# Optimization experiments

Measured on AMD Instinct MI355X. Metric: run time of the kernel, lower is better.

Reference implementation:

```python
import jax, jax.numpy as jnp
import numpy as np

D_MODEL, D_STATE, V_RANGE, IMG, K = 64, 16, 1, 32, 3
GROUPS = 4
EPS = 1e-5


def _gather_indices():
    H = W = IMG
    v_list = [(x, y) for x in range(-V_RANGE, V_RANGE + 1) for y in range(-V_RANGE, V_RANGE + 1)]
    idx = []
    yg, xg = np.meshgrid(np.arange(H), np.arange(W), indexing='ij')
    for vx, vy in v_list:
        src_y = (yg - vy) % H
        src_x = (xg - vx) % W
        idx.append((src_y * W + src_x).reshape(-1))
    return jnp.asarray(np.stack(idx, axis=0), dtype=jnp.int32)  # (V, H*W)


def setup_inputs() -> dict:
    key = jax.random.key(0)
    ks = jax.random.split(key, 8)
    B = 4
    V = (2 * V_RANGE + 1) ** 2
    fan = D_MODEL * K * K
    std = 1.0 / np.sqrt(fan)
    return {
        'u_t': jax.random.normal(ks[0], (B, D_MODEL, IMG, IMG), jnp.float32),
        's_prev': jax.random.normal(ks[1], (B, V, D_MODEL, D_STATE, IMG, IMG), jnp.float32),
        'gamma': jnp.ones((D_MODEL,), jnp.float32),
        'beta': jnp.zeros((D_MODEL,), jnp.float32),
        'w_delta': jax.random.uniform(ks[2], (D_MODEL, D_MODEL, K, K), jnp.float32, -std, std),
        'b_delta': jax.random.uniform(ks[3], (D_MODEL,), jnp.float32, -std, std),
        'w_B': jax.random.uniform(ks[4], (D_STATE, D_MODEL, K, K), jnp.float32, -std, std),
        'w_C': jax.random.uniform(ks[5], (D_STATE, D_MODEL, K, K), jnp.float32, -std, std),
        'log_A_real': jnp.log(0.5 * jnp.ones((D_MODEL, D_STATE), jnp.float32)),
        'D_param': jnp.ones((D_MODEL,), jnp.float32),
        'dt_inv_softplus': jnp.asarray(np.log(np.exp(1.0) - 1.0), jnp.float32),
        'gather_indices': _gather_indices(),
    }


def _group_norm(x, gamma, beta):
    B, D, H, W = x.shape
    xg = x.reshape(B, GROUPS, D // GROUPS, H, W)
    mu = xg.mean(axis=(2, 3, 4), keepdims=True)
    var = xg.var(axis=(2, 3, 4), keepdims=True)
    xn = ((xg - mu) / jnp.sqrt(var + EPS)).reshape(B, D, H, W)
    return xn * gamma[None, :, None, None] + beta[None, :, None, None]


def _circ_conv(x, w, b=None):
    p = K // 2
    xp = jnp.pad(x, ((0, 0), (0, 0), (p, p), (p, p)), mode='wrap')
    y = jax.lax.conv_general_dilated(xp, w, (1, 1), 'VALID',
                                     dimension_numbers=('NCHW', 'OIHW', 'NCHW'))
    if b is not None:
        y = y + b[None, :, None, None]
    return y


def reference(u_t, s_prev, gamma, beta, w_delta, b_delta, w_B, w_C,
              log_A_real, D_param, dt_inv_softplus, gather_indices):
    B, D, H, W = u_t.shape
    Bv, V, _, N, _, _ = s_prev.shape
    u_norm = _group_norm(u_t, gamma, beta)
    delta = jax.nn.softplus(_circ_conv(u_norm, w_delta, b_delta) + dt_inv_softplus)
    delta = jnp.clip(delta, 1e-4, 5.0)                      # (B,D,H,W)
    B_val = _circ_conv(u_norm, w_B)                          # (B,N,H,W)
    C_val = _circ_conv(u_norm, w_C)                          # (B,N,H,W)
    A = -jnp.exp(log_A_real)                                 # (D,N)
    A_bar = jnp.exp(delta[:, :, None] * A[None, :, :, None, None])  # (B,D,N,H,W)
    B_bar = delta[:, :, None] * B_val[:, None]               # (B,D,N,H,W)
    # flow transport: per-velocity periodic-shift gather over flattened HW
    s_flat = s_prev.reshape(B, V, D, N, H * W)
    s_trans = jax.vmap(lambda sv, iv: jnp.take(sv, iv, axis=-1),
                       in_axes=(1, 0), out_axes=1)(s_flat, gather_indices)
    s_trans = s_trans.reshape(B, V, D, N, H, W)
    s_new = A_bar[:, None] * s_trans + B_bar[:, None] * u_t[:, None, :, None]
    y_state = jnp.sum(s_new * C_val[:, None, None], axis=3)  # (B,V,D,H,W)
    y_new = y_state + u_t[:, None] * D_param[None, None, :, None, None]
    return (y_new, s_new)
```

## Files before the change

### kernel.cpp

```cpp
#include <hip/hip_runtime.h>
#include <hip/hip_bf16.h>

#define D_MODEL 64
#define D_STATE 16
#define IMG     32
#define HW      (IMG*IMG)
#define V       9
#define B       4
#define GROUPS  4
#define CPG     (D_MODEL/GROUPS)

typedef float f32x4 __attribute__((ext_vector_type(4)));

__global__ __launch_bounds__(256) void gn_kernel(
    const float* __restrict__ u, const float* __restrict__ gamma,
    const float* __restrict__ beta, float* __restrict__ un)
{
    const int b = blockIdx.x / GROUPS;
    const int g = blockIdx.x % GROUPS;
    const float* base = u + ((size_t)b*D_MODEL + g*CPG) * HW;
    const int NE = CPG * HW;

    float s = 0.f, s2 = 0.f;
    for (int i = threadIdx.x; i < NE; i += 256) {
        float v = base[i];
        s += v; s2 += v*v;
    }
    for (int off = 32; off; off >>= 1) {
        s  += __shfl_down(s,  off);
        s2 += __shfl_down(s2, off);
    }
    __shared__ float red0[4], red1[4];
    const int wave = threadIdx.x >> 6;
    if ((threadIdx.x & 63) == 0) { red0[wave] = s; red1[wave] = s2; }
    __syncthreads();
    if (threadIdx.x == 0) {
        float a = 0.f, c = 0.f;
        for (int i = 0; i < 4; i++) { a += red0[i]; c += red1[i]; }
        red0[0] = a; red1[0] = c;
    }
    __syncthreads();
    const float mean = red0[0] * (1.f/16384.f);
    const float var  = red1[0] * (1.f/16384.f) - mean*mean;
    const float rstd = rsqrtf(var + 1e-5f);

    for (int i = threadIdx.x; i < NE; i += 256) {
        int c = i >> 10;
        int d = g*CPG + c;
        float v = (base[i] - mean) * rstd;
        un[((size_t)b*D_MODEL + d)*HW + (i & (HW-1))] = v*gamma[d] + beta[d];
    }
}

__global__ __launch_bounds__(256) void aneg_kernel(
    const float* __restrict__ logA, float* __restrict__ aneg)
{
    int i = blockIdx.x*256 + threadIdx.x;
    if (i < D_MODEL*D_STATE) aneg[i] = -expf(logA[i]);
}

__global__ __launch_bounds__(256) void conv_kernel(
    const float* __restrict__ un,
    const float* __restrict__ w_delta, const float* __restrict__ b_delta,
    const float* __restrict__ w_B, const float* __restrict__ w_C,
    const float* __restrict__ dt_sp,
    float* __restrict__ delta, float* __restrict__ Bv, float* __restrict__ Cv)
{
    const int bx    = blockIdx.x;
    const int strip = bx & 3;
    const int cog   = (bx >> 2) % 24;
    const int b     = bx / 96;
    const int co0   = cog * 4;
    const int row0  = strip * 8;

    __shared__ float xs[16][10][32];
    __shared__ float wl[4][D_MODEL*9];

    for (int i = threadIdx.x; i < 4*D_MODEL*9; i += 256) {
        const int cl = i / (D_MODEL*9);
        const int rest = i % (D_MODEL*9);
        const int co = co0 + cl;
        const float* w = (co < 64) ? (w_delta + (size_t)co*(D_MODEL*9))
                       : (co < 80) ? (w_B + (size_t)(co-64)*(D_MODEL*9))
                                   : (w_C + (size_t)(co-80)*(D_MODEL*9));
        wl[cl][rest] = w[rest];
    }

    const int ly = threadIdx.x >> 5;
    const int ox = threadIdx.x & 31;
    const int oy = row0 + ly;

    const float* x = un + (size_t)b*D_MODEL*HW;
    float a0 = 0.f, a1 = 0.f, a2 = 0.f, a3 = 0.f;

    for (int c = 0; c < 4; c++) {
        __syncthreads();
        for (int i = threadIdx.x; i < 16*10*32; i += 256) {
            const int ci = i / 320;
            const int rr = (i % 320) >> 5;
            const int xx = i & 31;
            const int gy = (row0 - 1 + rr) & 31;
            xs[ci][rr][xx] = x[(size_t)(c*16 + ci)*HW + (gy << 5) + xx];
        }
        __syncthreads();

        #pragma unroll
        for (int ci = 0; ci < 16; ci++) {
            float v[3][3];
            #pragma unroll
            for (int dy = 0; dy < 3; dy++)
                #pragma unroll
                for (int dx = 0; dx < 3; dx++)
                    v[dy][dx] = xs[ci][ly + dy][(ox + dx + 31) & 31];
            const int cig = c*16 + ci;
            const float* w0 = &wl[0][cig*9];
            const float* w1 = &wl[1][cig*9];
            const float* w2 = &wl[2][cig*9];
            const float* w3 = &wl[3][cig*9];
            #pragma unroll
            for (int t = 0; t < 9; t++) {
                const float xv = v[t/3][t%3];
                a0 = fmaf(xv, w0[t], a0);
                a1 = fmaf(xv, w1[t], a1);
                a2 = fmaf(xv, w2[t], a2);
                a3 = fmaf(xv, w3[t], a3);
            }
        }
    }

    const int p = (oy << 5) + ox;
    const float dtsp = dt_sp[0];
    float accs[4] = {a0, a1, a2, a3};
    #pragma unroll
    for (int cl = 0; cl < 4; cl++) {
        const int co = co0 + cl;
        float acc = accs[cl];
        if (co < 64) {
            acc += b_delta[co] + dtsp;
            float sp = (acc > 15.f) ? acc : log1pf(__expf(acc));
            sp = fminf(fmaxf(sp, 1e-4f), 5.f);
            delta[((size_t)b*D_MODEL + co)*HW + p] = sp;
        } else if (co < 80) {
            Bv[((size_t)b*D_STATE + (co-64))*HW + p] = acc;
        } else {
            Cv[((size_t)b*D_STATE + (co-80))*HW + p] = acc;
        }
    }
}

template<int MODE>
__device__ __forceinline__ f32x4 rot4(const f32x4 own, int laneL, int laneR)
{
    f32x4 s;
    if (MODE == 0) {
        s = own;
    } else if (MODE == 1) {
        const float nb = __shfl(own.w, laneR, 64);
        s.x = own.y; s.y = own.z; s.z = own.w; s.w = nb;
    } else {
        const float nb = __shfl(own.w, laneL, 64);
        s.x = nb; s.y = own.x; s.z = own.y; s.w = own.z;
    }
    return s;
}

template<int MODE>
__device__ __forceinline__ void main_body(
    const float* __restrict__ sp_base, float* __restrict__ sn_base,
    const float* __restrict__ Bv_b, const float* __restrict__ Cv_b,
    const f32x4 dl, const f32x4 du, const float* an_,
    f32x4& y, int srcv, int p0, int laneL, int laneR)
{
    f32x4 sp[D_STATE], Bn[D_STATE], Cn[D_STATE];
    #pragma unroll
    for (int n = 0; n < D_STATE; n++)
        sp[n] = *(const f32x4*)(sp_base + n*HW + srcv);
    #pragma unroll
    for (int n = 0; n < D_STATE; n++)
        Bn[n] = *(const f32x4*)(Bv_b + n*HW);
    #pragma unroll
    for (int n = 0; n < D_STATE; n++)
        Cn[n] = *(const f32x4*)(Cv_b + n*HW);

    #pragma unroll
    for (int n = 0; n < D_STATE; n++) {
        f32x4 s;
        if (MODE == 0) {
            s = sp[n];
        } else if (MODE == 1) {
            const float nb = __shfl(sp[n].x, laneR, 64);
            s.x = sp[n].y; s.y = sp[n].z; s.z = sp[n].w; s.w = nb;
        } else {
            const float nb = __shfl(sp[n].w, laneL, 64);
            s.x = nb; s.y = sp[n].x; s.z = sp[n].y; s.w = sp[n].z;
        }
        const float anr = an_[n];
        f32x4 ab;
        ab.x = __expf(dl.x * anr);
        ab.y = __expf(dl.y * anr);
        ab.z = __expf(dl.z * anr);
        ab.w = __expf(dl.w * anr);
        const f32x4 sn = ab * s + du * Bn[n];
        __builtin_nontemporal_store(sn, (f32x4*)(sn_base + n*HW + p0));
        y += sn * Cn[n];
    }
}

__global__ __launch_bounds__(256, 2) void main_kernel(
    const float* __restrict__ sprev, const float* __restrict__ ut,
    const float* __restrict__ delta, const float* __restrict__ Bv,
    const float* __restrict__ Cv, const float* __restrict__ aneg,
    const float* __restrict__ Dp, const int* __restrict__ gidx,
    float* __restrict__ ynew, float* __restrict__ snew)
{
    const int blk = blockIdx.x;
    const int d   = blk % D_MODEL;
    const int tmp = blk / D_MODEL;
    const int v   = tmp % V;
    const int b   = tmp / V;

    const int t  = threadIdx.x;
    const int p0 = t * 4;
    const int y0 = p0 >> 5;
    const int x0 = p0 & 31;

    const int gi0 = gidx[v*HW];
    const int ryo = gi0 >> 5;
    const int rxo = gi0 & 31;

    const int ys   = (y0 + ryo) & 31;
    const int srcv = (ys << 5) + x0;

    const int lane  = t & 63;
    const int laneL = (lane & ~7) | ((lane + 7) & 7);
    const int laneR = (lane & ~7) | ((lane + 1) & 7);

    const size_t bvd = (((size_t)b*V + v)*D_MODEL + d);
    const float* sp_base = sprev + bvd * D_STATE * HW;
    float* sn_base = snew + bvd * D_STATE * HW;

    const float dpd = Dp[d];
    float an_[D_STATE];
    #pragma unroll
    for (int n = 0; n < D_STATE; n++) an_[n] = aneg[d*D_STATE + n];

    const f32x4 dl = *(const f32x4*)(delta + ((size_t)b*D_MODEL + d)*HW + p0);
    const f32x4 uu = *(const f32x4*)(ut    + ((size_t)b*D_MODEL + d)*HW + p0);
    const f32x4 du = dl * uu;
    const float* Bv_b = Bv + (size_t)b*D_STATE*HW + p0;
    const float* Cv_b = Cv + (size_t)b*D_STATE*HW + p0;

    f32x4 y = uu * dpd;

    if (rxo == 0) {
        main_body<0>(sp_base, sn_base, Bv_b, Cv_b, dl, du, an_, y, srcv, p0, laneL, laneR);
    } else if (rxo == 1) {
        main_body<1>(sp_base, sn_base, Bv_b, Cv_b, dl, du, an_, y, srcv, p0, laneL, laneR);
    } else if (rxo == 31) {
        main_body<2>(sp_base, sn_base, Bv_b, Cv_b, dl, du, an_, y, srcv, p0, laneL, laneR);
    } else {
        const int4 src4 = *(const int4*)(gidx + v*HW + p0);
        #pragma unroll
        for (int n = 0; n < D_STATE; n++) {
            const float* sp_n = sp_base + n*HW;
            const f32x4 Bn = *(const f32x4*)(Bv_b + n*HW);
            const f32x4 Cn = *(const f32x4*)(Cv_b + n*HW);
            const float anr = an_[n];
            f32x4 s;
            s.x = sp_n[src4.x]; s.y = sp_n[src4.y];
            s.z = sp_n[src4.z]; s.w = sp_n[src4.w];
            f32x4 ab;
            ab.x = __expf(dl.x * anr);
            ab.y = __expf(dl.y * anr);
            ab.z = __expf(dl.z * anr);
            ab.w = __expf(dl.w * anr);
            const f32x4 sn = ab * s + du * Bn;
            __builtin_nontemporal_store(sn, (f32x4*)(sn_base + n*HW + p0));
            y += sn * Cn;
        }
    }
    __builtin_nontemporal_store(y, (f32x4*)(ynew + bvd * HW + p0));
}

extern "C" void kernel_launch(void* const* d_in, const int* in_sizes, int n_in,
                              void* d_out, int out_size, void* d_ws, size_t ws_size,
                              hipStream_t stream)
{
    const float* u_t       = (const float*)d_in[0];
    const float* s_prev    = (const float*)d_in[1];
    const float* gamma     = (const float*)d_in[2];
    const float* beta      = (const float*)d_in[3];
    const float* w_delta   = (const float*)d_in[4];
    const float* b_delta   = (const float*)d_in[5];
    const float* w_B       = (const float*)d_in[6];
    const float* w_C       = (const float*)d_in[7];
    const float* log_A     = (const float*)d_in[8];
    const float* D_param   = (const float*)d_in[9];
    const float* dt_sp     = (const float*)d_in[10];
    const int*   gidx      = (const int*)d_in[11];

    float* ws = (float*)d_ws;
    float* un    = ws;
    float* delta = un    + (size_t)B*D_MODEL*HW;
    float* Bv    = delta + (size_t)B*D_MODEL*HW;
    float* Cv    = Bv    + (size_t)B*D_STATE*HW;
    float* aneg  = Cv    + (size_t)B*D_STATE*HW;

    float* ynew = (float*)d_out;
    float* snew = ynew + (size_t)B*V*D_MODEL*HW;

    gn_kernel<<<B*GROUPS, 256, 0, stream>>>(u_t, gamma, beta, un);
    aneg_kernel<<<(D_MODEL*D_STATE + 255)/256, 256, 0, stream>>>(log_A, aneg);
    conv_kernel<<<B*96, 256, 0, stream>>>(un, w_delta, b_delta, w_B, w_C, dt_sp,
                                          delta, Bv, Cv);
    main_kernel<<<B*V*D_MODEL, 256, 0, stream>>>(s_prev, u_t, delta, Bv, Cv,
                                                 aneg, D_param, gidx, ynew, snew);
}
```

Before: 103.9 us.

## Fold A negation into main kernel, interleave loads, use inline-asm streaming stores

Removes the separate aneg kernel and computes -exp(logA) inside the main kernel, saving one launch. The main body now loads state, B and C per iteration instead of prefetching all sixteen up front, which lowers register pressure. The launch-bounds occupancy hint is dropped. The s_new stores become inline assembly with sc0 sc1 nt cache bits, while the y_new store becomes a normal store. Interleaving loads with compute may expose more memory latency, and the inline asm bypasses compiler scheduling.

```diff
diff --git a/kernel.cpp b/kernel.cpp
--- a/kernel.cpp
+++ b/kernel.cpp
@@ -12,6 +12,11 @@
 
 typedef float f32x4 __attribute__((ext_vector_type(4)));
 
+__device__ __forceinline__ void stream_store4(float* p, f32x4 v) {
+    asm volatile("global_store_dwordx4 %0, %1, off sc0 sc1 nt"
+                 :: "v"(p), "v"(v) : "memory");
+}
+
 __global__ __launch_bounds__(256) void gn_kernel(
     const float* __restrict__ u, const float* __restrict__ gamma,
     const float* __restrict__ beta, float* __restrict__ un)
@@ -50,13 +55,6 @@
         float v = (base[i] - mean) * rstd;
         un[((size_t)b*D_MODEL + d)*HW + (i & (HW-1))] = v*gamma[d] + beta[d];
     }
-}
-
-__global__ __launch_bounds__(256) void aneg_kernel(
-    const float* __restrict__ logA, float* __restrict__ aneg)
-{
-    int i = blockIdx.x*256 + threadIdx.x;
-    if (i < D_MODEL*D_STATE) aneg[i] = -expf(logA[i]);
 }
 
 __global__ __launch_bounds__(256) void conv_kernel(
@@ -149,67 +147,43 @@
 }
 
 template<int MODE>
-__device__ __forceinline__ f32x4 rot4(const f32x4 own, int laneL, int laneR)
-{
-    f32x4 s;
-    if (MODE == 0) {
-        s = own;
-    } else if (MODE == 1) {
-        const float nb = __shfl(own.w, laneR, 64);
-        s.x = own.y; s.y = own.z; s.z = own.w; s.w = nb;
-    } else {
-        const float nb = __shfl(own.w, laneL, 64);
-        s.x = nb; s.y = own.x; s.z = own.y; s.w = own.z;
-    }
-    return s;
-}
-
-template<int MODE>
 __device__ __forceinline__ void main_body(
     const float* __restrict__ sp_base, float* __restrict__ sn_base,
     const float* __restrict__ Bv_b, const float* __restrict__ Cv_b,
     const f32x4 dl, const f32x4 du, const float* an_,
     f32x4& y, int srcv, int p0, int laneL, int laneR)
 {
-    f32x4 sp[D_STATE], Bn[D_STATE], Cn[D_STATE];
-    #pragma unroll
-    for (int n = 0; n < D_STATE; n++)
-        sp[n] = *(const f32x4*)(sp_base + n*HW + srcv);
-    #pragma unroll
-    for (int n = 0; n < D_STATE; n++)
-        Bn[n] = *(const f32x4*)(Bv_b + n*HW);
-    #pragma unroll
-    for (int n = 0; n < D_STATE; n++)
-        Cn[n] = *(const f32x4*)(Cv_b + n*HW);
-
     #pragma unroll
     for (int n = 0; n < D_STATE; n++) {
+        const f32x4 own = *(const f32x4*)(sp_base + n*HW + srcv);
         f32x4 s;
         if (MODE == 0) {
-            s = sp[n];
+            s = own;
         } else if (MODE == 1) {
-            const float nb = __shfl(sp[n].x, laneR, 64);
-            s.x = sp[n].y; s.y = sp[n].z; s.z = sp[n].w; s.w = nb;
+            const float nb = __shfl(own.x, laneR, 64);
+            s.x = own.y; s.y = own.z; s.z = own.w; s.w = nb;
         } else {
-            const float nb = __shfl(sp[n].w, laneL, 64);
-            s.x = nb; s.y = sp[n].x; s.z = sp[n].y; s.w = sp[n].z;
+            const float nb = __shfl(own.w, laneL, 64);
+            s.x = nb; s.y = own.x; s.z = own.y; s.w = own.z;
         }
         const float anr = an_[n];
+        const f32x4 Bn = *(const f32x4*)(Bv_b + n*HW);
+        const f32x4 Cn = *(const f32x4*)(Cv_b + n*HW);
         f32x4 ab;
         ab.x = __expf(dl.x * anr);
         ab.y = __expf(dl.y * anr);
         ab.z = __expf(dl.z * anr);
         ab.w = __expf(dl.w * anr);
-        const f32x4 sn = ab * s + du * Bn[n];
-        __builtin_nontemporal_store(sn, (f32x4*)(sn_base + n*HW + p0));
-        y += sn * Cn[n];
-    }
-}
-
-__global__ __launch_bounds__(256, 2) void main_kernel(
+        const f32x4 sn = ab * s + du * Bn;
+        stream_store4(sn_base + n*HW + p0, sn);
+        y += sn * Cn;
+    }
+}
+
+__global__ __launch_bounds__(256) void main_kernel(
     const float* __restrict__ sprev, const float* __restrict__ ut,
     const float* __restrict__ delta, const float* __restrict__ Bv,
-    const float* __restrict__ Cv, const float* __restrict__ aneg,
+    const float* __restrict__ Cv, const float* __restrict__ logA,
     const float* __restrict__ Dp, const int* __restrict__ gidx,
     float* __restrict__ ynew, float* __restrict__ snew)
 {
@@ -242,7 +216,7 @@
     const float dpd = Dp[d];
     float an_[D_STATE];
     #pragma unroll
-    for (int n = 0; n < D_STATE; n++) an_[n] = aneg[d*D_STATE + n];
+    for (int n = 0; n < D_STATE; n++) an_[n] = -__expf(logA[d*D_STATE + n]);
 
     const f32x4 dl = *(const f32x4*)(delta + ((size_t)b*D_MODEL + d)*HW + p0);
     const f32x4 uu = *(const f32x4*)(ut    + ((size_t)b*D_MODEL + d)*HW + p0);
@@ -275,11 +249,11 @@
             ab.z = __expf(dl.z * anr);
             ab.w = __expf(dl.w * anr);
             const f32x4 sn = ab * s + du * Bn;
-            __builtin_nontemporal_store(sn, (f32x4*)(sn_base + n*HW + p0));
+            stream_store4(sn_base + n*HW + p0, sn);
             y += sn * Cn;
         }
     }
-    __builtin_nontemporal_store(y, (f32x4*)(ynew + bvd * HW + p0));
+    *(f32x4*)(ynew + bvd * HW + p0) = y;
 }
 
 extern "C" void kernel_launch(void* const* d_in, const int* in_sizes, int n_in,
@@ -304,15 +278,13 @@
     float* delta = un    + (size_t)B*D_MODEL*HW;
     float* Bv    = delta + (size_t)B*D_MODEL*HW;
     float* Cv    = Bv    + (size_t)B*D_STATE*HW;
-    float* aneg  = Cv    + (size_t)B*D_STATE*HW;
 
     float* ynew = (float*)d_out;
     float* snew = ynew + (size_t)B*V*D_MODEL*HW;
 
     gn_kernel<<<B*GROUPS, 256, 0, stream>>>(u_t, gamma, beta, un);
-    aneg_kernel<<<(D_MODEL*D_STATE + 255)/256, 256, 0, stream>>>(log_A, aneg);
     conv_kernel<<<B*96, 256, 0, stream>>>(un, w_delta, b_delta, w_B, w_C, dt_sp,
                                           delta, Bv, Cv);
     main_kernel<<<B*V*D_MODEL, 256, 0, stream>>>(s_prev, u_t, delta, Bv, Cv,
-                                                 aneg, D_param, gidx, ynew, snew);
-}
+                                                 log_A, D_param, gidx, ynew, snew);
+}
```

New measurement: 106.8 us. +2.8%, slower.
